# Optimization experiments

Hardware: AMD Instinct MI355X
Metric: run time of the kernel (lower is better)

Reference implementation:

```python
import jax, jax.numpy as jnp
import numpy as np

B, T, I, H = 32768, 50, 2, 32  # batch, seq_len, input_size, hidden_size


def setup_inputs() -> dict:
    key = jax.random.key(0)
    ks = jax.random.split(key, 7)
    return {
        "x": jax.random.normal(ks[0], (B, T, I), dtype=jnp.float32),
        "W_ih": jax.random.normal(ks[1], (4 * H, I), dtype=jnp.float32) * 0.1,
        "W_hh": jax.random.normal(ks[2], (4 * H, H), dtype=jnp.float32) * 0.1,
        "b_ih": jax.random.normal(ks[3], (4 * H,), dtype=jnp.float32) * 0.1,
        "b_hh": jax.random.normal(ks[4], (4 * H,), dtype=jnp.float32) * 0.1,
        "W_out": jax.random.normal(ks[5], (1, H), dtype=jnp.float32) * 0.1,
        "b_out": jax.random.normal(ks[6], (1,), dtype=jnp.float32) * 0.1,
        "h0": jnp.zeros((B, H), dtype=jnp.float32),
        "c0": jnp.zeros((B, H), dtype=jnp.float32),
    }


def reference(x, W_ih, W_hh, b_ih, b_hh, W_out, b_out, h0, c0):
    # Precompute input projection for all timesteps: [B, T, 4H]
    xg = jnp.einsum("bti,gi->btg", x, W_ih) + b_ih + b_hh

    def step(carry, xg_t):
        h, c = carry  # [B, H] each
        gates = xg_t + h @ W_hh.T  # [B, 4H]
        i, f, g, o = jnp.split(gates, 4, axis=-1)  # PyTorch gate order i,f,g,o
        i = jax.nn.sigmoid(i)
        f = jax.nn.sigmoid(f)
        g = jnp.tanh(g)
        o = jax.nn.sigmoid(o)
        c = f * c + i * g
        h = o * jnp.tanh(c)
        return (h, c), h

    (_, _), hs = jax.lax.scan(step, (h0, c0), jnp.swapaxes(xg, 0, 1))  # hs: [T, B, H]
    r_out = jnp.swapaxes(hs, 0, 1)  # [B, T, H]
    results = r_out @ W_out.T + b_out  # [B, T, 1]
    return results.reshape(-1, 50, 1)
```

## Files before the change

### kernel.cpp

```cpp
#include <hip/hip_runtime.h>


#define TS 50
#define HSTR 36
#define CL 14.0f
#define WPB 4

typedef short short8 __attribute__((ext_vector_type(8)));
typedef float f32x4 __attribute__((ext_vector_type(4)));

__device__ __forceinline__ float fast_exp2(float x) {
    return __builtin_amdgcn_exp2f(x);
}
__device__ __forceinline__ float fast_rcp(float x) {
    return __builtin_amdgcn_rcpf(x);
}
__device__ __forceinline__ unsigned split_pack(float v) {
    unsigned u   = __float_as_uint(v);
    float    res = v - __uint_as_float(u & 0xffff0000u);
    return __builtin_amdgcn_perm(__float_as_uint(res), u, 0x07060302u);
}
__device__ __forceinline__ unsigned lo_pair(unsigned a, unsigned b) {
    return __builtin_amdgcn_perm(b, a, 0x05040100u);
}
__device__ __forceinline__ unsigned hi_pair(unsigned a, unsigned b) {
    return __builtin_amdgcn_perm(b, a, 0x07060302u);
}

union U4S8 { uint4 v; short8 s; unsigned u[4]; };

__global__ __launch_bounds__(256, 2)
void lsnn_kernel(const float* __restrict__ x,
                 const float* __restrict__ W_ih,
                 const float* __restrict__ W_hh,
                 const float* __restrict__ b_ih,
                 const float* __restrict__ b_hh,
                 const float* __restrict__ W_out,
                 const float* __restrict__ b_out,
                 const float* __restrict__ h0,
                 const float* __restrict__ c0,
                 float* __restrict__ out)
{
    __shared__ __align__(16) float    x_lds[WPB][16 * 100];
    __shared__ __align__(16) unsigned hpk[WPB][16 * HSTR];
    __shared__ __align__(16) float    out_lds[WPB][16 * TS];

    const int  g_w  = threadIdx.x >> 6;
    const int  lane = threadIdx.x & 63;
    const int  u0   = lane & 15;
    const int  q    = lane >> 4;
    const long b0   = ((long)blockIdx.x * WPB + g_w) * 16;

    float*    xw = x_lds[g_w];
    unsigned* hw = hpk[g_w];
    float*    ow = out_lds[g_w];

    {
        const float4* xs = (const float4*)(x + b0 * 100);
        float4* xd = (float4*)xw;
        for (int i = lane; i < 400; i += 64) xd[i] = xs[i];
    }
    for (int i = lane; i < 512; i += 64) {
        int r = i >> 5, u = i & 31;
        hw[r * HSTR + u] = split_pack(h0[b0 * 32 + i]);
    }

    const float L2E = 1.4426950408889634f;
    const float SG  = 2.0f * L2E;

    short8 Bh[8], Bl[8];
    float  wx0[8], wx1[8], bias[8];
    #pragma unroll
    for (int n = 0; n < 8; ++n) {
        const float s = ((n >> 1) == 2) ? (2.0f * L2E) : -L2E;
        const int   gg = n * 16 + u0;
        const float* wr = W_hh + gg * 32 + q * 8;
        U4S8 uh, ul;
        #pragma unroll
        for (int p = 0; p < 4; ++p) {
            unsigned p0 = split_pack(wr[2*p]   * s);
            unsigned p1 = split_pack(wr[2*p+1] * s);
            uh.u[p] = lo_pair(p0, p1);
            ul.u[p] = hi_pair(p0, p1);
        }
        Bh[n] = uh.s;  Bl[n] = ul.s;
        wx0[n]  = W_ih[gg * 2 + 0] * s;
        wx1[n]  = W_ih[gg * 2 + 1] * s;
        bias[n] = (b_ih[gg] + b_hh[gg]) * s;
    }
    short8 Bwh, Bwl;
    {
        U4S8 uh, ul;
        #pragma unroll
        for (int p = 0; p < 4; ++p) {
            unsigned p0 = split_pack(W_out[q * 8 + 2*p]);
            unsigned p1 = split_pack(W_out[q * 8 + 2*p + 1]);
            uh.u[p] = lo_pair(p0, p1);
            ul.u[p] = hi_pair(p0, p1);
        }
        Bwh = uh.s;  Bwl = ul.s;
    }
    const float bout = b_out[0];

    float cst[8];
    #pragma unroll
    for (int hu = 0; hu < 2; ++hu)
        #pragma unroll
        for (int r = 0; r < 4; ++r)
            cst[hu * 4 + r] = c0[(b0 + q * 4 + r) * 32 + hu * 16 + u0];

    const f32x4 ZV = {0.f, 0.f, 0.f, 0.f};
    const int abase = u0 * HSTR + q * 8;

    float2 xv[4];
    #pragma unroll
    for (int r = 0; r < 4; ++r)
        xv[r] = *(const float2*)&xw[(q * 4 + r) * 100];

    #pragma unroll 1
    for (int t = 0; t < TS; ++t) {
        uint4 hq0 = *(const uint4*)&hw[abase];
        uint4 hq1 = *(const uint4*)&hw[abase + 4];
        U4S8 Ahh, Ahl;
        Ahh.u[0] = lo_pair(hq0.x, hq0.y); Ahh.u[1] = lo_pair(hq0.z, hq0.w);
        Ahh.u[2] = lo_pair(hq1.x, hq1.y); Ahh.u[3] = lo_pair(hq1.z, hq1.w);
        Ahl.u[0] = hi_pair(hq0.x, hq0.y); Ahl.u[1] = hi_pair(hq0.z, hq0.w);
        Ahl.u[2] = hi_pair(hq1.x, hq1.y); Ahl.u[3] = hi_pair(hq1.z, hq1.w);

        if (t > 0) {
            f32x4 aw = ZV;
            aw = __builtin_amdgcn_mfma_f32_16x16x32_bf16(Ahh.s, Bwh, aw, 0, 0, 0);
            aw = __builtin_amdgcn_mfma_f32_16x16x32_bf16(Ahl.s, Bwh, aw, 0, 0, 0);
            aw = __builtin_amdgcn_mfma_f32_16x16x32_bf16(Ahh.s, Bwl, aw, 0, 0, 0);
            if (u0 == 0) {
                #pragma unroll
                for (int r = 0; r < 4; ++r)
                    ow[(q * 4 + r) * TS + (t - 1)] = aw[r] + bout;
            }
        }

        f32x4 acc[8];
        #pragma unroll
        for (int n = 0; n < 8; ++n) {
            f32x4 ci;
            #pragma unroll
            for (int r = 0; r < 4; ++r)
                ci[r] = fmaf(wx1[n], xv[r].y, fmaf(wx0[n], xv[r].x, bias[n]));
            acc[n] = __builtin_amdgcn_mfma_f32_16x16x32_bf16(Ahh.s, Bh[n], ci,     0, 0, 0);
            acc[n] = __builtin_amdgcn_mfma_f32_16x16x32_bf16(Ahl.s, Bh[n], acc[n], 0, 0, 0);
            acc[n] = __builtin_amdgcn_mfma_f32_16x16x32_bf16(Ahh.s, Bl[n], acc[n], 0, 0, 0);
        }

        if (t + 1 < TS) {
            #pragma unroll
            for (int r = 0; r < 4; ++r)
                xv[r] = *(const float2*)&xw[(q * 4 + r) * 100 + 2 * (t + 1)];
        }

        float Bvs[8], Cvs[8], abps[8], epvs[8], pps[8];
        #pragma unroll
        for (int s = 0; s < 8; ++s) {
            const int hu = s >> 2, r = s & 3;
            float zi = acc[0 + hu][r];
            float zf = acc[2 + hu][r];
            float zg = fminf(acc[4 + hu][r], CL);
            float zo = acc[6 + hu][r];
            float Av = fast_exp2(zi);
            Bvs[s]   = fast_exp2(zg);
            float Ev = fast_exp2(zf);
            Cvs[s]   = fast_exp2(zo);
            float Ap = 1.0f + Av, Bp = 1.0f + Bvs[s];
            epvs[s]  = 1.0f + Ev;
            abps[s]  = Ap * Bp;
            pps[s]   = abps[s] * epvs[s];
        }
        float rgs[8];
        #pragma unroll
        for (int s = 0; s < 4; ++s) {
            float pr = pps[s] * pps[s + 4];
            float ri = fast_rcp(pr);
            rgs[s]     = pps[s + 4] * ri;
            rgs[s + 4] = pps[s]     * ri;
        }
        float Dvs[8], qvs[8];
        #pragma unroll
        for (int s = 0; s < 8; ++s) {
            float fv = abps[s] * rgs[s];
            float ig = (Bvs[s] - 1.0f) * (epvs[s] * rgs[s]);
            float c  = fmaf(fv, cst[s], ig);
            cst[s] = c;
            Dvs[s] = fast_exp2(fminf(SG * c, CL));
            qvs[s] = (1.0f + Cvs[s]) * (1.0f + Dvs[s]);
        }
        float rqs[8];
        #pragma unroll
        for (int s = 0; s < 4; ++s) {
            float qr = qvs[s] * qvs[s + 4];
            float ri = fast_rcp(qr);
            rqs[s]     = qvs[s + 4] * ri;
            rqs[s + 4] = qvs[s]     * ri;
        }
        #pragma unroll
        for (int s = 0; s < 8; ++s) {
            const int hu = s >> 2, r = s & 3;
            float h = (Dvs[s] - 1.0f) * rqs[s];
            hw[(q * 4 + r) * HSTR + hu * 16 + u0] = split_pack(h);
        }
    }

    {
        uint4 hq0 = *(const uint4*)&hw[abase];
        uint4 hq1 = *(const uint4*)&hw[abase + 4];
        U4S8 Ahh, Ahl;
        Ahh.u[0] = lo_pair(hq0.x, hq0.y); Ahh.u[1] = lo_pair(hq0.z, hq0.w);
        Ahh.u[2] = lo_pair(hq1.x, hq1.y); Ahh.u[3] = lo_pair(hq1.z, hq1.w);
        Ahl.u[0] = hi_pair(hq0.x, hq0.y); Ahl.u[1] = hi_pair(hq0.z, hq0.w);
        Ahl.u[2] = hi_pair(hq1.x, hq1.y); Ahl.u[3] = hi_pair(hq1.z, hq1.w);
        f32x4 aw = {0.f, 0.f, 0.f, 0.f};
        aw = __builtin_amdgcn_mfma_f32_16x16x32_bf16(Ahh.s, Bwh, aw, 0, 0, 0);
        aw = __builtin_amdgcn_mfma_f32_16x16x32_bf16(Ahl.s, Bwh, aw, 0, 0, 0);
        aw = __builtin_amdgcn_mfma_f32_16x16x32_bf16(Ahh.s, Bwl, aw, 0, 0, 0);
        if (u0 == 0) {
            #pragma unroll
            for (int r = 0; r < 4; ++r)
                ow[(q * 4 + r) * TS + 49] = aw[r] + bout;
        }
    }

    {
        float4* od = (float4*)(out + b0 * 50);
        const float4* os = (const float4*)ow;
        for (int i = lane; i < 200; i += 64) od[i] = os[i];
    }
}

extern "C" void kernel_launch(void* const* d_in, const int* in_sizes, int n_in,
                              void* d_out, int out_size, void* d_ws, size_t ws_size,
                              hipStream_t stream) {
    const float* x     = (const float*)d_in[0];
    const float* W_ih  = (const float*)d_in[1];
    const float* W_hh  = (const float*)d_in[2];
    const float* b_ih  = (const float*)d_in[3];
    const float* b_hh  = (const float*)d_in[4];
    const float* W_out = (const float*)d_in[5];
    const float* b_out = (const float*)d_in[6];
    const float* h0    = (const float*)d_in[7];
    const float* c0    = (const float*)d_in[8];
    float* out = (float*)d_out;

    dim3 grid(32768 / (16 * WPB)), block(64 * WPB);
    lsnn_kernel<<<grid, block, 0, stream>>>(x, W_ih, W_hh, b_ih, b_hh,
                                            W_out, b_out, h0, c0, out);
}
```

Measured before the change: 164.1 us.

## Process two 16-row batch groups per wavefront to interleave independent recurrences

Each single-wave block now handles 32 batch rows as two independent 16-row groups, interleaving their MFMA chains and gate math within one wavefront. Blocks shrink from four waves to one, and the grid covers the batch with half as many wavefronts. The aim is to hide MFMA and transcendental latency on the serial timestep chain through instruction-level parallelism. In exchange, register pressure roughly doubles (launch bounds now 64,1), which may lower occupancy and leave fewer waves per CU to hide latency.

```diff
diff --git a/kernel.cpp b/kernel.cpp
--- a/kernel.cpp
+++ b/kernel.cpp
@@ -4,7 +4,6 @@
 #define TS 50
 #define HSTR 36
 #define CL 14.0f
-#define WPB 4
 
 typedef short short8 __attribute__((ext_vector_type(8)));
 typedef float f32x4 __attribute__((ext_vector_type(4)));
@@ -29,7 +28,7 @@
 
 union U4S8 { uint4 v; short8 s; unsigned u[4]; };
 
-__global__ __launch_bounds__(256, 2)
+__global__ __launch_bounds__(64, 1)
 void lsnn_kernel(const float* __restrict__ x,
                  const float* __restrict__ W_ih,
                  const float* __restrict__ W_hh,
@@ -41,28 +40,23 @@
                  const float* __restrict__ c0,
                  float* __restrict__ out)
 {
-    __shared__ __align__(16) float    x_lds[WPB][16 * 100];
-    __shared__ __align__(16) unsigned hpk[WPB][16 * HSTR];
-    __shared__ __align__(16) float    out_lds[WPB][16 * TS];
-
-    const int  g_w  = threadIdx.x >> 6;
-    const int  lane = threadIdx.x & 63;
+    __shared__ __align__(16) float    x_lds[2][16 * 100];
+    __shared__ __align__(16) unsigned hpk[2][16 * HSTR];
+    __shared__ __align__(16) float    out_lds[2][16 * TS];
+
+    const int  lane = threadIdx.x;
     const int  u0   = lane & 15;
     const int  q    = lane >> 4;
-    const long b0   = ((long)blockIdx.x * WPB + g_w) * 16;
-
-    float*    xw = x_lds[g_w];
-    unsigned* hw = hpk[g_w];
-    float*    ow = out_lds[g_w];
+    const long b0   = (long)blockIdx.x * 32;
 
     {
         const float4* xs = (const float4*)(x + b0 * 100);
-        float4* xd = (float4*)xw;
-        for (int i = lane; i < 400; i += 64) xd[i] = xs[i];
-    }
-    for (int i = lane; i < 512; i += 64) {
-        int r = i >> 5, u = i & 31;
-        hw[r * HSTR + u] = split_pack(h0[b0 * 32 + i]);
+        float4* xd = (float4*)&x_lds[0][0];
+        for (int i = lane; i < 800; i += 64) xd[i] = xs[i];
+    }
+    for (int i = lane; i < 1024; i += 64) {
+        int g = i >> 9, r = (i >> 5) & 15, u = i & 31;
+        hpk[g][r * HSTR + u] = split_pack(h0[b0 * 32 + i]);
     }
 
     const float L2E = 1.4426950408889634f;
@@ -102,69 +96,87 @@
     }
     const float bout = b_out[0];
 
-    float cst[8];
-    #pragma unroll
-    for (int hu = 0; hu < 2; ++hu)
-        #pragma unroll
-        for (int r = 0; r < 4; ++r)
-            cst[hu * 4 + r] = c0[(b0 + q * 4 + r) * 32 + hu * 16 + u0];
+    float cst[2][8];
+    #pragma unroll
+    for (int g = 0; g < 2; ++g)
+        #pragma unroll
+        for (int hu = 0; hu < 2; ++hu)
+            #pragma unroll
+            for (int r = 0; r < 4; ++r)
+                cst[g][hu * 4 + r] =
+                    c0[(b0 + g * 16 + q * 4 + r) * 32 + hu * 16 + u0];
 
     const f32x4 ZV = {0.f, 0.f, 0.f, 0.f};
     const int abase = u0 * HSTR + q * 8;
 
-    float2 xv[4];
-    #pragma unroll
-    for (int r = 0; r < 4; ++r)
-        xv[r] = *(const float2*)&xw[(q * 4 + r) * 100];
+    float2 xv[2][4];
+    #pragma unroll
+    for (int g = 0; g < 2; ++g)
+        #pragma unroll
+        for (int r = 0; r < 4; ++r)
+            xv[g][r] = *(const float2*)&x_lds[g][(q * 4 + r) * 100];
 
     #pragma unroll 1
     for (int t = 0; t < TS; ++t) {
-        uint4 hq0 = *(const uint4*)&hw[abase];
-        uint4 hq1 = *(const uint4*)&hw[abase + 4];
-        U4S8 Ahh, Ahl;
-        Ahh.u[0] = lo_pair(hq0.x, hq0.y); Ahh.u[1] = lo_pair(hq0.z, hq0.w);
-        Ahh.u[2] = lo_pair(hq1.x, hq1.y); Ahh.u[3] = lo_pair(hq1.z, hq1.w);
-        Ahl.u[0] = hi_pair(hq0.x, hq0.y); Ahl.u[1] = hi_pair(hq0.z, hq0.w);
-        Ahl.u[2] = hi_pair(hq1.x, hq1.y); Ahl.u[3] = hi_pair(hq1.z, hq1.w);
+        U4S8 Ahh[2], Ahl[2];
+        #pragma unroll
+        for (int g = 0; g < 2; ++g) {
+            uint4 hq0 = *(const uint4*)&hpk[g][abase];
+            uint4 hq1 = *(const uint4*)&hpk[g][abase + 4];
+            Ahh[g].u[0] = lo_pair(hq0.x, hq0.y); Ahh[g].u[1] = lo_pair(hq0.z, hq0.w);
+            Ahh[g].u[2] = lo_pair(hq1.x, hq1.y); Ahh[g].u[3] = lo_pair(hq1.z, hq1.w);
+            Ahl[g].u[0] = hi_pair(hq0.x, hq0.y); Ahl[g].u[1] = hi_pair(hq0.z, hq0.w);
+            Ahl[g].u[2] = hi_pair(hq1.x, hq1.y); Ahl[g].u[3] = hi_pair(hq1.z, hq1.w);
+        }
 
         if (t > 0) {
-            f32x4 aw = ZV;
-            aw = __builtin_amdgcn_mfma_f32_16x16x32_bf16(Ahh.s, Bwh, aw, 0, 0, 0);
-            aw = __builtin_amdgcn_mfma_f32_16x16x32_bf16(Ahl.s, Bwh, aw, 0, 0, 0);
-            aw = __builtin_amdgcn_mfma_f32_16x16x32_bf16(Ahh.s, Bwl, aw, 0, 0, 0);
-            if (u0 == 0) {
+            #pragma unroll
+            for (int g = 0; g < 2; ++g) {
+                f32x4 aw = ZV;
+                aw = __builtin_amdgcn_mfma_f32_16x16x32_bf16(Ahh[g].s, Bwh, aw, 0, 0, 0);
+                aw = __builtin_amdgcn_mfma_f32_16x16x32_bf16(Ahl[g].s, Bwh, aw, 0, 0, 0);
+                aw = __builtin_amdgcn_mfma_f32_16x16x32_bf16(Ahh[g].s, Bwl, aw, 0, 0, 0);
+                if (u0 == 0) {
+                    #pragma unroll
+                    for (int r = 0; r < 4; ++r)
+                        out_lds[g][(q * 4 + r) * TS + (t - 1)] = aw[r] + bout;
+                }
+            }
+        }
+
+        f32x4 acc[2][8];
+        #pragma unroll
+        for (int n = 0; n < 8; ++n) {
+            #pragma unroll
+            for (int g = 0; g < 2; ++g) {
+                f32x4 ci;
                 #pragma unroll
                 for (int r = 0; r < 4; ++r)
-                    ow[(q * 4 + r) * TS + (t - 1)] = aw[r] + bout;
+                    ci[r] = fmaf(wx1[n], xv[g][r].y,
+                                 fmaf(wx0[n], xv[g][r].x, bias[n]));
+                acc[g][n] = __builtin_amdgcn_mfma_f32_16x16x32_bf16(Ahh[g].s, Bh[n], ci,        0, 0, 0);
+                acc[g][n] = __builtin_amdgcn_mfma_f32_16x16x32_bf16(Ahl[g].s, Bh[n], acc[g][n], 0, 0, 0);
+                acc[g][n] = __builtin_amdgcn_mfma_f32_16x16x32_bf16(Ahh[g].s, Bl[n], acc[g][n], 0, 0, 0);
             }
         }
 
-        f32x4 acc[8];
-        #pragma unroll
-        for (int n = 0; n < 8; ++n) {
-            f32x4 ci;
-            #pragma unroll
-            for (int r = 0; r < 4; ++r)
-                ci[r] = fmaf(wx1[n], xv[r].y, fmaf(wx0[n], xv[r].x, bias[n]));
-            acc[n] = __builtin_amdgcn_mfma_f32_16x16x32_bf16(Ahh.s, Bh[n], ci,     0, 0, 0);
-            acc[n] = __builtin_amdgcn_mfma_f32_16x16x32_bf16(Ahl.s, Bh[n], acc[n], 0, 0, 0);
-            acc[n] = __builtin_amdgcn_mfma_f32_16x16x32_bf16(Ahh.s, Bl[n], acc[n], 0, 0, 0);
-        }
-
         if (t + 1 < TS) {
             #pragma unroll
-            for (int r = 0; r < 4; ++r)
-                xv[r] = *(const float2*)&xw[(q * 4 + r) * 100 + 2 * (t + 1)];
-        }
-
-        float Bvs[8], Cvs[8], abps[8], epvs[8], pps[8];
-        #pragma unroll
-        for (int s = 0; s < 8; ++s) {
-            const int hu = s >> 2, r = s & 3;
-            float zi = acc[0 + hu][r];
-            float zf = acc[2 + hu][r];
-            float zg = fminf(acc[4 + hu][r], CL);
-            float zo = acc[6 + hu][r];
+            for (int g = 0; g < 2; ++g)
+                #pragma unroll
+                for (int r = 0; r < 4; ++r)
+                    xv[g][r] = *(const float2*)
+                        &x_lds[g][(q * 4 + r) * 100 + 2 * (t + 1)];
+        }
+
+        float Bvs[16], Cvs[16], abps[16], epvs[16], pps[16];
+        #pragma unroll
+        for (int s = 0; s < 16; ++s) {
+            const int g = s >> 3, hu = (s >> 2) & 1, r = s & 3;
+            float zi = acc[g][0 + hu][r];
+            float zf = acc[g][2 + hu][r];
+            float zg = fminf(acc[g][4 + hu][r], CL);
+            float zo = acc[g][6 + hu][r];
             float Av = fast_exp2(zi);
             Bvs[s]   = fast_exp2(zg);
             float Ev = fast_exp2(zf);
@@ -174,43 +186,45 @@
             abps[s]  = Ap * Bp;
             pps[s]   = abps[s] * epvs[s];
         }
-        float rgs[8];
-        #pragma unroll
-        for (int s = 0; s < 4; ++s) {
-            float pr = pps[s] * pps[s + 4];
+        float rgs[16];
+        #pragma unroll
+        for (int s = 0; s < 8; ++s) {
+            float pr = pps[s] * pps[s + 8];
             float ri = fast_rcp(pr);
-            rgs[s]     = pps[s + 4] * ri;
-            rgs[s + 4] = pps[s]     * ri;
-        }
-        float Dvs[8], qvs[8];
-        #pragma unroll
-        for (int s = 0; s < 8; ++s) {
+            rgs[s]     = pps[s + 8] * ri;
+            rgs[s + 8] = pps[s]     * ri;
+        }
+        float Dvs[16], qvs[16];
+        #pragma unroll
+        for (int s = 0; s < 16; ++s) {
+            const int g = s >> 3;
             float fv = abps[s] * rgs[s];
             float ig = (Bvs[s] - 1.0f) * (epvs[s] * rgs[s]);
-            float c  = fmaf(fv, cst[s], ig);
-            cst[s] = c;
+            float c  = fmaf(fv, cst[g][s & 7], ig);
+            cst[g][s & 7] = c;
             Dvs[s] = fast_exp2(fminf(SG * c, CL));
             qvs[s] = (1.0f + Cvs[s]) * (1.0f + Dvs[s]);
         }
-        float rqs[8];
-        #pragma unroll
-        for (int s = 0; s < 4; ++s) {
-            float qr = qvs[s] * qvs[s + 4];
+        float rqs[16];
+        #pragma unroll
+        for (int s = 0; s < 8; ++s) {
+            float qr = qvs[s] * qvs[s + 8];
             float ri = fast_rcp(qr);
-            rqs[s]     = qvs[s + 4] * ri;
-            rqs[s + 4] = qvs[s]     * ri;
-        }
-        #pragma unroll
-        for (int s = 0; s < 8; ++s) {
-            const int hu = s >> 2, r = s & 3;
+            rqs[s]     = qvs[s + 8] * ri;
+            rqs[s + 8] = qvs[s]     * ri;
+        }
+        #pragma unroll
+        for (int s = 0; s < 16; ++s) {
+            const int g = s >> 3, hu = (s >> 2) & 1, r = s & 3;
             float h = (Dvs[s] - 1.0f) * rqs[s];
-            hw[(q * 4 + r) * HSTR + hu * 16 + u0] = split_pack(h);
-        }
-    }
-
-    {
-        uint4 hq0 = *(const uint4*)&hw[abase];
-        uint4 hq1 = *(const uint4*)&hw[abase + 4];
+            hpk[g][(q * 4 + r) * HSTR + hu * 16 + u0] = split_pack(h);
+        }
+    }
+
+    #pragma unroll
+    for (int g = 0; g < 2; ++g) {
+        uint4 hq0 = *(const uint4*)&hpk[g][abase];
+        uint4 hq1 = *(const uint4*)&hpk[g][abase + 4];
         U4S8 Ahh, Ahl;
         Ahh.u[0] = lo_pair(hq0.x, hq0.y); Ahh.u[1] = lo_pair(hq0.z, hq0.w);
         Ahh.u[2] = lo_pair(hq1.x, hq1.y); Ahh.u[3] = lo_pair(hq1.z, hq1.w);
@@ -223,14 +237,14 @@
         if (u0 == 0) {
             #pragma unroll
             for (int r = 0; r < 4; ++r)
-                ow[(q * 4 + r) * TS + 49] = aw[r] + bout;
+                out_lds[g][(q * 4 + r) * TS + 49] = aw[r] + bout;
         }
     }
 
     {
         float4* od = (float4*)(out + b0 * 50);
-        const float4* os = (const float4*)ow;
-        for (int i = lane; i < 200; i += 64) od[i] = os[i];
+        const float4* os = (const float4*)&out_lds[0][0];
+        for (int i = lane; i < 400; i += 64) od[i] = os[i];
     }
 }
 
@@ -248,7 +262,7 @@
     const float* c0    = (const float*)d_in[8];
     float* out = (float*)d_out;
 
-    dim3 grid(32768 / (16 * WPB)), block(64 * WPB);
+    dim3 grid(32768 / 32), block(64);
     lsnn_kernel<<<grid, block, 0, stream>>>(x, W_ih, W_hh, b_ih, b_hh,
                                             W_out, b_out, h0, c0, out);
 }
```

Measured after the change: 190.3 us. +15.9%, slower.
